# Optimization experiments

Hardware: AMD Instinct MI355X
Metric: run time of the kernel (lower is better)

## Reference

```python
import jax, jax.numpy as jnp
import numpy as np
import math

B, S_IN, S_OUT, D_IN, D_OUT, G = 8, 1024, 1024, 96, 96, 8
LN_EPS = 1e-5


def setup_inputs() -> dict:
    key = jax.random.key(0)
    k_x, k_m, k_p, k_l = jax.random.split(key, 4)
    x = jax.random.normal(k_x, (B, S_IN, D_IN), dtype=jnp.float32)
    M = jax.random.uniform(k_m, (D_OUT, D_IN), minval=-0.5, maxval=0.5, dtype=jnp.float32)
    P = jax.random.uniform(k_p, (D_OUT, D_OUT, G), minval=-0.1, maxval=0.1, dtype=jnp.float32)
    Linker = jax.random.uniform(k_l, (S_IN, S_OUT), minval=-0.1, maxval=0.1, dtype=jnp.float32)
    gamma = jnp.ones((D_OUT,), dtype=jnp.float32)
    beta = jnp.zeros((D_OUT,), dtype=jnp.float32)
    return {"x": x, "M": M, "P": P, "Linker": Linker, "gamma": gamma, "beta": beta}


def _layer_norm(z, gamma, beta):
    mu = jnp.mean(z, axis=-1, keepdims=True)
    var = jnp.mean(jnp.square(z - mu), axis=-1, keepdims=True)
    return (z - mu) * jax.lax.rsqrt(var + LN_EPS) * gamma + beta


def reference(x, M, P, Linker, gamma, beta):
    # Z = x @ M^T, then LayerNorm over feature dim
    Z0 = jnp.einsum('bsj,ij->bsi', x, M)           # (B, S_in, D_out)
    Z = _layer_norm(Z0, gamma, beta)
    # periods[i,j,g] = i*(D_out*G) + j*G + g + 2
    periods = (jnp.arange(D_OUT * D_OUT * G, dtype=jnp.float32)
               .reshape(D_OUT, D_OUT, G) + 2.0)
    k = jnp.arange(S_IN, dtype=jnp.float32)
    # phi[s,i,j,g] = cos(2*pi*s / periods[i,j,g])
    phi = jnp.cos((2.0 * math.pi) * k[:, None, None, None] / periods[None])
    # fuse basis reduction: W[s,i,j] = sum_g P[i,j,g] * phi[s,i,j,g]
    W = jnp.einsum('sijg,ijg->sij', phi, P)        # (S_in, D_out, D_out)
    # T[b,s,i] = sum_j Z[b,s,j] * W[s,i,j]
    T = jnp.einsum('bsj,sij->bsi', Z, W)           # (B, S_in, D_out)
    # sequence transform via Linker
    U = jnp.einsum('bsi,st->bti', T, Linker)       # (B, S_out, D_out)
    # shared residual: x @ M^T (pre-LN) through the same Linker
    residual = jnp.einsum('bsi,st->bti', Z0, Linker)
    return U + residual
```

## Files before the change

### kernel.cpp

```cpp
#include <hip/hip_runtime.h>
#include <cstdint>
#include <cstddef>

#define NPAIR 9216
#define BSTRIDE 98304

typedef __attribute__((ext_vector_type(8))) short short8;
typedef __attribute__((ext_vector_type(4))) float f32x4;

__device__ __forceinline__ uint16_t f2bf(float x) {
    uint32_t u = __float_as_uint(x);
    return (uint16_t)((u + 0x7FFF + ((u >> 16) & 1)) >> 16);
}
__device__ __forceinline__ float bf2f(uint16_t b) {
    return __uint_as_float(((uint32_t)b) << 16);
}

union SmemK1 {
    struct { float zb[2][32][100]; float ps[2][32][3][2]; float stats[2][32][2]; } ln;
    struct { float T[64][17]; } kl;
};

__global__ __launch_bounds__(256) void k1_mega(
    const float* __restrict__ x, const float* __restrict__ M,
    const float* __restrict__ P, const float* __restrict__ L,
    const float* __restrict__ gamma, const float* __restrict__ beta,
    float* __restrict__ Z0, float* __restrict__ Z,
    uint16_t* __restrict__ Lt, uint16_t* __restrict__ Wt)
{
    __shared__ SmemK1 sm;
    const int t  = threadIdx.x;
    const int bx = blockIdx.x;

    if (bx < 128) {
        const int g = t >> 7, lt = t & 127;
        const int R0 = bx * 64 + g * 32;
        if (lt < 96) {
            float mreg[96];
            #pragma unroll
            for (int k4 = 0; k4 < 24; ++k4) {
                float4 v = *(const float4*)(M + lt * 96 + k4 * 4);
                mreg[k4*4+0]=v.x; mreg[k4*4+1]=v.y;
                mreg[k4*4+2]=v.z; mreg[k4*4+3]=v.w;
            }
            for (int r = 0; r < 32; ++r) {
                const float* xr = x + (size_t)(R0 + r) * 96;
                float a0 = 0.f, a1 = 0.f, a2 = 0.f, a3 = 0.f;
                #pragma unroll
                for (int j = 0; j < 96; j += 4) {
                    a0 = fmaf(xr[j+0], mreg[j+0], a0);
                    a1 = fmaf(xr[j+1], mreg[j+1], a1);
                    a2 = fmaf(xr[j+2], mreg[j+2], a2);
                    a3 = fmaf(xr[j+3], mreg[j+3], a3);
                }
                float z = (a0 + a1) + (a2 + a3);
                sm.ln.zb[g][r][lt] = z;
                Z0[(size_t)(R0 + r) * 96 + lt] = z;
            }
        }
        __syncthreads();
        if (lt < 96) {
            int row = lt / 3, seg = lt % 3;
            const float4* zp = (const float4*)&sm.ln.zb[g][row][seg * 32];
            float s1 = 0.f, s2 = 0.f;
            #pragma unroll
            for (int k = 0; k < 8; ++k) {
                float4 v = zp[k];
                s1 += (v.x + v.y) + (v.z + v.w);
                s2 += (v.x*v.x + v.y*v.y) + (v.z*v.z + v.w*v.w);
            }
            sm.ln.ps[g][row][seg][0] = s1;
            sm.ln.ps[g][row][seg][1] = s2;
        }
        __syncthreads();
        if (lt < 32) {
            float s1 = sm.ln.ps[g][lt][0][0] + sm.ln.ps[g][lt][1][0] + sm.ln.ps[g][lt][2][0];
            float s2 = sm.ln.ps[g][lt][0][1] + sm.ln.ps[g][lt][1][1] + sm.ln.ps[g][lt][2][1];
            float mu  = s1 * (1.f / 96.f);
            float var = s2 * (1.f / 96.f) - mu * mu;
            sm.ln.stats[g][lt][0] = mu;
            sm.ln.stats[g][lt][1] = rsqrtf(var + 1e-5f);
        }
        __syncthreads();
        if (lt < 96) {
            float gm = gamma[lt], bt = beta[lt];
            for (int r = 0; r < 32; ++r) {
                float mu = sm.ln.stats[g][r][0], rs = sm.ln.stats[g][r][1];
                Z[(size_t)(R0 + r) * 96 + lt] = (sm.ln.zb[g][r][lt] - mu) * rs * gm + bt;
            }
        }
        return;
    }

    if (bx < 144) {
        for (int cgi = 0; cgi < 4; ++cgi) {
            const int t0 = (bx - 128) * 64 + cgi * 16;
            const int tx = t & 15, ty = t >> 4;
            for (int s0 = 0; s0 < 1024; s0 += 64) {
                #pragma unroll
                for (int k = 0; k < 4; ++k) {
                    int sr = ty + k * 16;
                    sm.kl.T[sr][tx] = L[(size_t)(s0 + sr) * 1024 + t0 + tx];
                }
                __syncthreads();
                {
                    int trow = t >> 4, sc = (t & 15) * 4;
                    uint32_t u01 = (uint32_t)f2bf(sm.kl.T[sc+0][trow]) |
                                   ((uint32_t)f2bf(sm.kl.T[sc+1][trow]) << 16);
                    uint32_t u23 = (uint32_t)f2bf(sm.kl.T[sc+2][trow]) |
                                   ((uint32_t)f2bf(sm.kl.T[sc+3][trow]) << 16);
                    uint2 o; o.x = u01; o.y = u23;
                    *(uint2*)(Lt + (size_t)(t0 + trow) * 1024 + s0 + sc) = o;
                }
                __syncthreads();
            }
        }
        return;
    }

    {
        const int u  = (bx - 144) * 256 + t;
        const int p  = u % 9216;
        const int sc = u / 9216;
        const int i  = p % 96, j = p / 96;
        const int s0 = sc * 64;
        const int base = (i * 96 + j) * 8;

        float Pv[8], c[8], cp[8], tc1[8];
        {
            float4 a = *(const float4*)(P + base);
            float4 b = *(const float4*)(P + base + 4);
            Pv[0]=a.x; Pv[1]=a.y; Pv[2]=a.z; Pv[3]=a.w;
            Pv[4]=b.x; Pv[5]=b.y; Pv[6]=b.z; Pv[7]=b.w;
        }
        #pragma unroll
        for (int g = 0; g < 8; ++g) {
            float inv = 1.0f / (float)(base + g + 2);
            float c1  = cospif(2.0f * inv);
            tc1[g] = c1 + c1;
            c[g]  = cospif(2.0f * (float)s0 * inv);
            cp[g] = cospif(2.0f * (float)(s0 - 1) * inv);
        }
        uint16_t* op = Wt + (size_t)s0 * NPAIR + p;
        for (int ss = 0; ss < 64; ++ss) {
            float w = 0.f;
            #pragma unroll
            for (int g = 0; g < 8; ++g) w = fmaf(Pv[g], c[g], w);
            *op = f2bf(w);
            op += NPAIR;
            #pragma unroll
            for (int g = 0; g < 8; ++g) {
                float cn = fmaf(tc1[g], c[g], -cp[g]);
                cp[g] = c[g]; c[g] = cn;
            }
        }
    }
}

__global__ __launch_bounds__(96) void kt_apply(
    const float* __restrict__ Z, const float* __restrict__ Z0,
    const uint16_t* __restrict__ Wt, uint16_t* __restrict__ Vt)
{
    const int i  = threadIdx.x;
    const int s  = blockIdx.x >> 1;
    const int b0 = (blockIdx.x & 1) * 4;
    float acc[4] = {0.f, 0.f, 0.f, 0.f};
    const uint16_t* wrow = Wt + (size_t)s * NPAIR + i;
    const float* zs = Z + (size_t)b0 * BSTRIDE + (size_t)s * 96;
    #pragma unroll 8
    for (int j = 0; j < 96; ++j) {
        float w = bf2f(wrow[j * 96]);
        #pragma unroll
        for (int bb = 0; bb < 4; ++bb)
            acc[bb] = fmaf(zs[(size_t)bb * BSTRIDE + j], w, acc[bb]);
    }
    #pragma unroll
    for (int bb = 0; bb < 4; ++bb) {
        size_t o = (size_t)(b0 + bb) * BSTRIDE + (size_t)s * 96 + i;
        Vt[((size_t)(b0 + bb) * 96 + i) * 1024 + s] = f2bf(acc[bb] + Z0[o]);
    }
}

__global__ __launch_bounds__(256) void k3_mfma(
    const uint16_t* __restrict__ Lt, const uint16_t* __restrict__ Vt,
    float* __restrict__ out)
{
    __shared__ float red[4][64][25];
    const int lane = threadIdx.x & 63;
    const int wv   = threadIdx.x >> 6;
    const int m    = lane & 15;
    const int quad = lane >> 4;
    const int t0   = blockIdx.x * 16;
    const int b    = blockIdx.y;

    const uint16_t* Lp = Lt + (size_t)(t0 + m) * 1024 + wv * 256 + quad * 8;
    const uint16_t* Vp = Vt + ((size_t)b * 96 + m) * 1024 + wv * 256 + quad * 8;

    f32x4 acc[6];
    #pragma unroll
    for (int ii = 0; ii < 6; ++ii) acc[ii] = (f32x4){0.f, 0.f, 0.f, 0.f};

    short8 a = *(const short8*)Lp;
    short8 bv[6];
    #pragma unroll
    for (int ii = 0; ii < 6; ++ii)
        bv[ii] = *(const short8*)(Vp + (size_t)ii * 16 * 1024);

    for (int kc = 0; kc < 7; ++kc) {
        short8 an = *(const short8*)(Lp + (kc + 1) * 32);
        short8 bn[6];
        #pragma unroll
        for (int ii = 0; ii < 6; ++ii)
            bn[ii] = *(const short8*)(Vp + (size_t)ii * 16 * 1024 + (kc + 1) * 32);
        #pragma unroll
        for (int ii = 0; ii < 6; ++ii)
            acc[ii] = __builtin_amdgcn_mfma_f32_16x16x32_bf16(a, bv[ii], acc[ii], 0, 0, 0);
        a = an;
        #pragma unroll
        for (int ii = 0; ii < 6; ++ii) bv[ii] = bn[ii];
    }
    #pragma unroll
    for (int ii = 0; ii < 6; ++ii)
        acc[ii] = __builtin_amdgcn_mfma_f32_16x16x32_bf16(a, bv[ii], acc[ii], 0, 0, 0);

    #pragma unroll
    for (int ii = 0; ii < 6; ++ii)
        #pragma unroll
        for (int r = 0; r < 4; ++r)
            red[wv][lane][ii * 4 + r] = acc[ii][r];
    __syncthreads();
    {
        const int l2 = threadIdx.x & 63;
        const int ks = (threadIdx.x >> 6) * 6;
        const int m2 = l2 & 15, q2 = l2 >> 4;
        #pragma unroll
        for (int k = ks; k < ks + 6; ++k) {
            float sv = red[0][l2][k] + red[1][l2][k]
                     + red[2][l2][k] + red[3][l2][k];
            int ii = k >> 2, r = k & 3;
            out[(size_t)b * BSTRIDE + (size_t)(t0 + q2 * 4 + r) * 96 + ii * 16 + m2] = sv;
        }
    }
}

extern "C" void kernel_launch(void* const* d_in, const int* in_sizes, int n_in,
                              void* d_out, int out_size, void* d_ws, size_t ws_size,
                              hipStream_t stream)
{
    const float* x     = (const float*)d_in[0];
    const float* M     = (const float*)d_in[1];
    const float* P     = (const float*)d_in[2];
    const float* Lnk   = (const float*)d_in[3];
    const float* gamma = (const float*)d_in[4];
    const float* beta  = (const float*)d_in[5];
    float* out = (float*)d_out;

    uint8_t* ws = (uint8_t*)d_ws;
    uint16_t* Wt = (uint16_t*)ws;
    float*    Z0 = (float*)(ws + 18874368);
    float*    Z  = (float*)(ws + 22020096);
    uint16_t* Lt = (uint16_t*)(ws + 25165824);
    uint16_t* Vt = (uint16_t*)(ws + 27262976);

    k1_mega <<<720,  256, 0, stream>>>(x, M, P, Lnk, gamma, beta, Z0, Z, Lt, Wt);
    kt_apply<<<2048, 96,  0, stream>>>(Z, Z0, Wt, Vt);
    k3_mfma <<<dim3(64, 8), 256, 0, stream>>>(Lt, Vt, out);
}
```

Before: 131.5 us.

## Rebalance mega-kernel block roles and parallelize Linker transpose across many blocks

```diff
diff --git a/kernel.cpp b/kernel.cpp
--- a/kernel.cpp
+++ b/kernel.cpp
@@ -18,7 +18,7 @@
 
 union SmemK1 {
     struct { float zb[2][32][100]; float ps[2][32][3][2]; float stats[2][32][2]; } ln;
-    struct { float T[64][17]; } kl;
+    struct { float T[64][65]; } kl;
 };
 
 __global__ __launch_bounds__(256) void k1_mega(
@@ -32,9 +32,48 @@
     const int t  = threadIdx.x;
     const int bx = blockIdx.x;
 
-    if (bx < 128) {
+    if (bx < 576) {
+        const int u  = bx * 256 + t;
+        const int p  = u % 9216;
+        const int sc = u / 9216;
+        const int i  = p % 96, j = p / 96;
+        const int s0 = sc * 64;
+        const int base = (i * 96 + j) * 8;
+
+        float Pv[8], c[8], cp[8], tc1[8];
+        {
+            float4 a = *(const float4*)(P + base);
+            float4 b = *(const float4*)(P + base + 4);
+            Pv[0]=a.x; Pv[1]=a.y; Pv[2]=a.z; Pv[3]=a.w;
+            Pv[4]=b.x; Pv[5]=b.y; Pv[6]=b.z; Pv[7]=b.w;
+        }
+        #pragma unroll
+        for (int g = 0; g < 8; ++g) {
+            float inv = 1.0f / (float)(base + g + 2);
+            float c1  = cospif(2.0f * inv);
+            tc1[g] = c1 + c1;
+            c[g]  = cospif(2.0f * (float)s0 * inv);
+            cp[g] = cospif(2.0f * (float)(s0 - 1) * inv);
+        }
+        uint16_t* op = Wt + (size_t)s0 * NPAIR + p;
+        for (int ss = 0; ss < 64; ++ss) {
+            float w = 0.f;
+            #pragma unroll
+            for (int g = 0; g < 8; ++g) w = fmaf(Pv[g], c[g], w);
+            *op = f2bf(w);
+            op += NPAIR;
+            #pragma unroll
+            for (int g = 0; g < 8; ++g) {
+                float cn = fmaf(tc1[g], c[g], -cp[g]);
+                cp[g] = c[g]; c[g] = cn;
+            }
+        }
+        return;
+    }
+
+    if (bx < 704) {
         const int g = t >> 7, lt = t & 127;
-        const int R0 = bx * 64 + g * 32;
+        const int R0 = (bx - 576) * 64 + g * 32;
         if (lt < 96) {
             float mreg[96];
             #pragma unroll
@@ -92,78 +131,40 @@
         return;
     }
 
-    if (bx < 144) {
-        for (int cgi = 0; cgi < 4; ++cgi) {
-            const int t0 = (bx - 128) * 64 + cgi * 16;
-            const int tx = t & 15, ty = t >> 4;
-            for (int s0 = 0; s0 < 1024; s0 += 64) {
-                #pragma unroll
-                for (int k = 0; k < 4; ++k) {
-                    int sr = ty + k * 16;
-                    sm.kl.T[sr][tx] = L[(size_t)(s0 + sr) * 1024 + t0 + tx];
-                }
-                __syncthreads();
-                {
-                    int trow = t >> 4, sc = (t & 15) * 4;
-                    uint32_t u01 = (uint32_t)f2bf(sm.kl.T[sc+0][trow]) |
-                                   ((uint32_t)f2bf(sm.kl.T[sc+1][trow]) << 16);
-                    uint32_t u23 = (uint32_t)f2bf(sm.kl.T[sc+2][trow]) |
-                                   ((uint32_t)f2bf(sm.kl.T[sc+3][trow]) << 16);
-                    uint2 o; o.x = u01; o.y = u23;
-                    *(uint2*)(Lt + (size_t)(t0 + trow) * 1024 + s0 + sc) = o;
-                }
-                __syncthreads();
-            }
-        }
-        return;
-    }
-
     {
-        const int u  = (bx - 144) * 256 + t;
-        const int p  = u % 9216;
-        const int sc = u / 9216;
-        const int i  = p % 96, j = p / 96;
-        const int s0 = sc * 64;
-        const int base = (i * 96 + j) * 8;
-
-        float Pv[8], c[8], cp[8], tc1[8];
+        const int tau = bx - 704;
+        const int s0 = (tau & 15) * 64, t0 = (tau >> 4) * 64;
+        #pragma unroll
+        for (int k = 0; k < 16; ++k) {
+            int mi = t + 256 * k;
+            int sr = mi >> 6, c = mi & 63;
+            sm.kl.T[sr][c] = L[(size_t)(s0 + sr) * 1024 + t0 + c];
+        }
+        __syncthreads();
         {
-            float4 a = *(const float4*)(P + base);
-            float4 b = *(const float4*)(P + base + 4);
-            Pv[0]=a.x; Pv[1]=a.y; Pv[2]=a.z; Pv[3]=a.w;
-            Pv[4]=b.x; Pv[5]=b.y; Pv[6]=b.z; Pv[7]=b.w;
-        }
-        #pragma unroll
-        for (int g = 0; g < 8; ++g) {
-            float inv = 1.0f / (float)(base + g + 2);
-            float c1  = cospif(2.0f * inv);
-            tc1[g] = c1 + c1;
-            c[g]  = cospif(2.0f * (float)s0 * inv);
-            cp[g] = cospif(2.0f * (float)(s0 - 1) * inv);
-        }
-        uint16_t* op = Wt + (size_t)s0 * NPAIR + p;
-        for (int ss = 0; ss < 64; ++ss) {
-            float w = 0.f;
-            #pragma unroll
-            for (int g = 0; g < 8; ++g) w = fmaf(Pv[g], c[g], w);
-            *op = f2bf(w);
-            op += NPAIR;
-            #pragma unroll
-            for (int g = 0; g < 8; ++g) {
-                float cn = fmaf(tc1[g], c[g], -cp[g]);
-                cp[g] = c[g]; c[g] = cn;
-            }
-        }
-    }
-}
-
-__global__ __launch_bounds__(96) void kt_apply(
+            const int trow = t >> 2, sc0 = (t & 3) * 16;
+            uint32_t w[8];
+            #pragma unroll
+            for (int q = 0; q < 8; ++q) {
+                w[q] = (uint32_t)f2bf(sm.kl.T[sc0 + 2*q][trow]) |
+                       ((uint32_t)f2bf(sm.kl.T[sc0 + 2*q + 1][trow]) << 16);
+            }
+            uint16_t* ob = Lt + (size_t)(t0 + trow) * 1024 + s0 + sc0;
+            uint4 o0; o0.x = w[0]; o0.y = w[1]; o0.z = w[2]; o0.w = w[3];
+            uint4 o1; o1.x = w[4]; o1.y = w[5]; o1.z = w[6]; o1.w = w[7];
+            *(uint4*)ob = o0;
+            *(uint4*)(ob + 8) = o1;
+        }
+    }
+}
+
+__global__ __launch_bounds__(192) void kt_apply(
     const float* __restrict__ Z, const float* __restrict__ Z0,
     const uint16_t* __restrict__ Wt, uint16_t* __restrict__ Vt)
 {
-    const int i  = threadIdx.x;
-    const int s  = blockIdx.x >> 1;
-    const int b0 = (blockIdx.x & 1) * 4;
+    const int i  = threadIdx.x % 96;
+    const int b0 = (threadIdx.x / 96) * 4;
+    const int s  = blockIdx.x;
     float acc[4] = {0.f, 0.f, 0.f, 0.f};
     const uint16_t* wrow = Wt + (size_t)s * NPAIR + i;
     const float* zs = Z + (size_t)b0 * BSTRIDE + (size_t)s * 96;
@@ -262,7 +263,7 @@
     uint16_t* Lt = (uint16_t*)(ws + 25165824);
     uint16_t* Vt = (uint16_t*)(ws + 27262976);
 
-    k1_mega <<<720,  256, 0, stream>>>(x, M, P, Lnk, gamma, beta, Z0, Z, Lt, Wt);
-    kt_apply<<<2048, 96,  0, stream>>>(Z, Z0, Wt, Vt);
+    k1_mega <<<960,  256, 0, stream>>>(x, M, P, Lnk, gamma, beta, Z0, Z, Lt, Wt);
+    kt_apply<<<1024, 192, 0, stream>>>(Z, Z0, Wt, Vt);
     k3_mfma <<<dim3(64, 8), 256, 0, stream>>>(Lt, Vt, out);
 }
```

New measurement: 143.5 us. 9.1% more time.
